# Kernel optimization log

Measured on AMD Instinct MI355X. Metric: run time of the kernel, lower is better.

Reference implementation:

```python
import jax, jax.numpy as jnp
import numpy as np

B, S, H = 4, 4096, 2048
E = 64          # num_routed_experts
TOP_K = 8
TEMP = 1.0      # router_temperature


def setup_inputs() -> dict:
    key = jax.random.key(0)
    k1, k2 = jax.random.split(key)
    hidden_states = jax.random.normal(k1, (B, S, H), dtype=jnp.float32)
    # nn.Linear weight: [out_features, in_features] = [E, H]
    gate_w = jax.random.normal(k2, (E, H), dtype=jnp.float32) * (1.0 / np.sqrt(H))
    return {"hidden_states": hidden_states, "gate_w": gate_w}


def reference(hidden_states, gate_w):
    # Gate projection + temperature scaling: [B,S,H] @ [H,E] -> [B,S,E]
    router_logits = jnp.einsum("bsh,eh->bse", hidden_states, gate_w) / TEMP
    # Top-k over experts
    routing_weights, selected_experts = jax.lax.top_k(router_logits, TOP_K)
    # Softmax over the top-k slots in fp32, cast back to input dtype
    routing_weights = jax.nn.softmax(routing_weights.astype(jnp.float32), axis=-1).astype(hidden_states.dtype)
    return router_logits, routing_weights, selected_experts
```

## Files before the change

kernel.cpp:

```cpp
#include <hip/hip_runtime.h>
#include <math.h>

#define HH 2048
#define EE 64
#define TOPK 8
#define NT 16384
#define MT 32
#define KC 16
#define KQR 512
#define NCH 32
#define LS 68

typedef __attribute__((ext_vector_type(8)))  short short8;
typedef __attribute__((ext_vector_type(16))) float f32x16;

static __device__ __forceinline__ void cvt3(const float4& a, const float4& b,
                                            short8& h, short8& m, short8& l)
{
    const float v[8] = {a.x, a.y, a.z, a.w, b.x, b.y, b.z, b.w};
#pragma unroll
    for (int i = 0; i < 8; ++i) {
        const unsigned int u = __float_as_uint(v[i]);
        h[i] = (short)(u >> 16);
        const float r1 = v[i] - __uint_as_float(u & 0xffff0000u);
        const unsigned int u1 = __float_as_uint(r1);
        m[i] = (short)(u1 >> 16);
        const float r2 = r1 - __uint_as_float(u1 & 0xffff0000u);
        const unsigned int u2 = __float_as_uint(r2);
        l[i] = (short)((u2 + 0x7fffu + ((u2 >> 16) & 1u)) >> 16);
    }
}

__global__ __launch_bounds__(256) void wsplit(
    const float* __restrict__ w, short* __restrict__ wsw)
{
    const int e = blockIdx.x;
    const int o = threadIdx.x;
    const int k = o * 8;
    const float4 a = *(const float4*)(w + (size_t)e * HH + k);
    const float4 b = *(const float4*)(w + (size_t)e * HH + k + 4);
    short8 h, m, l;
    cvt3(a, b, h, m, l);

    const int eb = e >> 5, lr = e & 31;
    const int kq = k >> 9;
    const int c  = (k >> 4) & 31;
    const int l5 = (k >> 3) & 1;
    const int lane = l5 * 32 + lr;
    short* dst = wsw + ((size_t)(((eb * 4 + kq) * 32 + c) * 3) * 64 + lane) * 8;
    *(short8*)(dst)            = h;
    *(short8*)(dst + 64 * 8)   = m;
    *(short8*)(dst + 128 * 8)  = l;
}

__global__ __launch_bounds__(512, 4) void router_fused(
    const float* __restrict__ x,
    const short* __restrict__ wsw,
    float* __restrict__ out_logits,
    float* __restrict__ out_wts,
    float* __restrict__ out_idx)
{
    __shared__ float slog[MT * LS];

    const int t    = threadIdx.x;
    const int wv   = t >> 6;
    const int lane = t & 63;
    const int eb   = wv & 1;
    const int kq   = wv >> 1;
    const int l5   = lane >> 5;
    const int lr   = lane & 31;
    const int tok0 = blockIdx.x * MT;

    const float* xp = x + (size_t)(tok0 + lr) * HH + kq * KQR + l5 * 8;
    const short* wbase = wsw + ((size_t)((eb * 4 + kq) * 32) * 192 + lane) * 8;

    f32x16 accM = {0}, accS = {0};

    short8 wA[3], wB[3];
    float4 xa0, xa1, xb0, xb1;

    auto wload = [&](short8* bw, int c) {
        const short* p0 = wbase + (size_t)c * 1536;
        bw[0] = *(const short8*)(p0);
        bw[1] = *(const short8*)(p0 + 512);
        bw[2] = *(const short8*)(p0 + 1024);
    };
    auto xload = [&](float4& a, float4& b, int c) {
        a = *(const float4*)(xp + c * KC);
        b = *(const float4*)(xp + c * KC + 4);
    };
    auto compute = [&](const float4& a, const float4& b, const short8* bw) {
        short8 xh, xm, xl;
        cvt3(a, b, xh, xm, xl);
        accM = __builtin_amdgcn_mfma_f32_32x32x16_bf16(xh, bw[0], accM, 0, 0, 0);
        accS = __builtin_amdgcn_mfma_f32_32x32x16_bf16(xh, bw[1], accS, 0, 0, 0);
        accS = __builtin_amdgcn_mfma_f32_32x32x16_bf16(xm, bw[0], accS, 0, 0, 0);
        accS = __builtin_amdgcn_mfma_f32_32x32x16_bf16(xh, bw[2], accS, 0, 0, 0);
        accS = __builtin_amdgcn_mfma_f32_32x32x16_bf16(xl, bw[0], accS, 0, 0, 0);
        accS = __builtin_amdgcn_mfma_f32_32x32x16_bf16(xm, bw[1], accS, 0, 0, 0);
    };

    wload(wA, 0); xload(xa0, xa1, 0);
    wload(wB, 1); xload(xb0, xb1, 1);

#pragma unroll 1
    for (int c = 0; c < NCH; c += 2) {
        compute(xa0, xa1, wA);
        if (c + 2 < NCH) { wload(wA, c + 2); xload(xa0, xa1, c + 2); }
        compute(xb0, xb1, wB);
        if (c + 3 < NCH) { wload(wB, c + 3); xload(xb0, xb1, c + 3); }
    }

    const int col = eb * 32 + lr;
#pragma unroll 1
    for (int q = 0; q < 4; ++q) {
        if (kq == q) {
#pragma unroll
            for (int r = 0; r < 16; ++r) {
                const int row = (r & 3) + 8 * (r >> 2) + 4 * l5;
                const float val = accM[r] + accS[r];
                if (q == 0) slog[row * LS + col] = val;
                else        slog[row * LS + col] += val;
            }
        }
        __syncthreads();
    }

    {
        const int row = t >> 4;
        const int c4  = (t & 15) * 4;
        const float4 o0 = *(const float4*)&slog[row * LS + c4];
        *(float4*)(out_logits + (size_t)(tok0 + row) * EE + c4) = o0;
    }

    if (t < MT) {
        float tv[TOPK];
        int   ti[TOPK];
#pragma unroll
        for (int q = 0; q < TOPK; ++q) { tv[q] = -INFINITY; ti[q] = 0; }

        for (int e = 0; e < EE; ++e) {
            const float val = slog[t * LS + e];
            if (val > tv[TOPK - 1]) {
                tv[TOPK - 1] = val;
                ti[TOPK - 1] = e;
#pragma unroll
                for (int q = TOPK - 1; q > 0; --q) {
                    if (tv[q] > tv[q - 1]) {
                        float fv = tv[q]; tv[q] = tv[q - 1]; tv[q - 1] = fv;
                        int   fi = ti[q]; ti[q] = ti[q - 1]; ti[q - 1] = fi;
                    }
                }
            }
        }

        const float m = tv[0];
        float ew[TOPK];
        float sum = 0.f;
#pragma unroll
        for (int q = 0; q < TOPK; ++q) { ew[q] = expf(tv[q] - m); sum += ew[q]; }
        const float inv = 1.f / sum;

        const size_t tok = (size_t)(tok0 + t);
        float4 w0, w1, i0, i1;
        w0.x = ew[0] * inv; w0.y = ew[1] * inv; w0.z = ew[2] * inv; w0.w = ew[3] * inv;
        w1.x = ew[4] * inv; w1.y = ew[5] * inv; w1.z = ew[6] * inv; w1.w = ew[7] * inv;
        i0.x = (float)ti[0]; i0.y = (float)ti[1]; i0.z = (float)ti[2]; i0.w = (float)ti[3];
        i1.x = (float)ti[4]; i1.y = (float)ti[5]; i1.z = (float)ti[6]; i1.w = (float)ti[7];
        *(float4*)(out_wts + tok * TOPK)     = w0;
        *(float4*)(out_wts + tok * TOPK + 4) = w1;
        *(float4*)(out_idx + tok * TOPK)     = i0;
        *(float4*)(out_idx + tok * TOPK + 4) = i1;
    }
}

extern "C" void kernel_launch(void* const* d_in, const int* in_sizes, int n_in,
                              void* d_out, int out_size, void* d_ws, size_t ws_size,
                              hipStream_t stream) {
    const float* x = (const float*)d_in[0];
    const float* w = (const float*)d_in[1];
    float* out        = (float*)d_out;
    float* out_logits = out;
    float* out_wts    = out + (size_t)NT * EE;
    float* out_idx    = out_wts + (size_t)NT * TOPK;
    short* wsw = (short*)d_ws;

    hipLaunchKernelGGL(wsplit, dim3(EE), dim3(256), 0, stream, w, wsw);
    hipLaunchKernelGGL(router_fused, dim3(NT / MT), dim3(512), 0, stream,
                       x, wsw, out_logits, out_wts, out_idx);
}
```

Baseline: 233.8 us.

## Stage x tiles in shared memory so fp32 split is done once per tile

Before, the two expert-half waves that share a k-quarter each loaded x and ran the three-way bf16 split themselves, so every x element was converted twice. Now all 512 threads cooperatively load a 128-wide K chunk of x, split it once, and store the three parts in a double-buffered, XOR-swizzled LDS tile. Waves read their MFMA A operands from LDS, and the weight layout is reorganised into 16-wide K slices to match. The cost is a __syncthreads per chunk and LDS traffic in place of register-resident x, which may reduce how well global loads overlap with MFMA work.

```diff
diff --git a/kernel.cpp b/kernel.cpp
--- a/kernel.cpp
+++ b/kernel.cpp
@@ -6,9 +6,8 @@
 #define TOPK 8
 #define NT 16384
 #define MT 32
-#define KC 16
-#define KQR 512
-#define NCH 32
+#define KC 128
+#define NCH 16
 #define LS 68
 
 typedef __attribute__((ext_vector_type(8)))  short short8;
@@ -42,15 +41,14 @@
     short8 h, m, l;
     cvt3(a, b, h, m, l);
 
-    const int eb = e >> 5, lr = e & 31;
-    const int kq = k >> 9;
-    const int c  = (k >> 4) & 31;
-    const int l5 = (k >> 3) & 1;
+    const int eb  = e >> 5, lr = e & 31;
+    const int s16 = o >> 1;
+    const int l5  = o & 1;
     const int lane = l5 * 32 + lr;
-    short* dst = wsw + ((size_t)(((eb * 4 + kq) * 32 + c) * 3) * 64 + lane) * 8;
-    *(short8*)(dst)            = h;
-    *(short8*)(dst + 64 * 8)   = m;
-    *(short8*)(dst + 128 * 8)  = l;
+    short* dst = wsw + (((size_t)(eb * 128 + s16) * 3) * 64 + lane) * 8;
+    *(short8*)(dst)           = h;
+    *(short8*)(dst + 64 * 8)  = m;
+    *(short8*)(dst + 128 * 8) = l;
 }
 
 __global__ __launch_bounds__(512, 4) void router_fused(
@@ -60,7 +58,8 @@
     float* __restrict__ out_wts,
     float* __restrict__ out_idx)
 {
-    __shared__ float slog[MT * LS];
+    __shared__ __align__(16) short8 xsl[2][1536];
+    float* slog = (float*)xsl;
 
     const int t    = threadIdx.x;
     const int wv   = t >> 6;
@@ -71,44 +70,60 @@
     const int lr   = lane & 31;
     const int tok0 = blockIdx.x * MT;
 
-    const float* xp = x + (size_t)(tok0 + lr) * HH + kq * KQR + l5 * 8;
-    const short* wbase = wsw + ((size_t)((eb * 4 + kq) * 32) * 192 + lane) * 8;
+    const int sr = t >> 4;
+    const int su = t & 15;
+    const float* xg = x + (size_t)(tok0 + sr) * HH + su * 8;
+    const int s16s = su >> 1;
+    const int lfs  = (su & 1) * 32 + sr;
 
     f32x16 accM = {0}, accS = {0};
-
-    short8 wA[3], wB[3];
-    float4 xa0, xa1, xb0, xb1;
-
-    auto wload = [&](short8* bw, int c) {
-        const short* p0 = wbase + (size_t)c * 1536;
-        bw[0] = *(const short8*)(p0);
-        bw[1] = *(const short8*)(p0 + 512);
-        bw[2] = *(const short8*)(p0 + 1024);
+    float4 xr0, xr1;
+
+    auto sload = [&](int c) {
+        xr0 = *(const float4*)(xg + (size_t)c * KC);
+        xr1 = *(const float4*)(xg + (size_t)c * KC + 4);
     };
-    auto xload = [&](float4& a, float4& b, int c) {
-        a = *(const float4*)(xp + c * KC);
-        b = *(const float4*)(xp + c * KC + 4);
+    auto swrite = [&](int buf) {
+        short8 h, m, l;
+        cvt3(xr0, xr1, h, m, l);
+        const int b0 = s16s * 3;
+        xsl[buf][((b0 + 0) << 6) + (lfs ^ ((b0 + 0) & 7))] = h;
+        xsl[buf][((b0 + 1) << 6) + (lfs ^ ((b0 + 1) & 7))] = m;
+        xsl[buf][((b0 + 2) << 6) + (lfs ^ ((b0 + 2) & 7))] = l;
     };
-    auto compute = [&](const float4& a, const float4& b, const short8* bw) {
-        short8 xh, xm, xl;
-        cvt3(a, b, xh, xm, xl);
-        accM = __builtin_amdgcn_mfma_f32_32x32x16_bf16(xh, bw[0], accM, 0, 0, 0);
-        accS = __builtin_amdgcn_mfma_f32_32x32x16_bf16(xh, bw[1], accS, 0, 0, 0);
-        accS = __builtin_amdgcn_mfma_f32_32x32x16_bf16(xm, bw[0], accS, 0, 0, 0);
-        accS = __builtin_amdgcn_mfma_f32_32x32x16_bf16(xh, bw[2], accS, 0, 0, 0);
-        accS = __builtin_amdgcn_mfma_f32_32x32x16_bf16(xl, bw[0], accS, 0, 0, 0);
-        accS = __builtin_amdgcn_mfma_f32_32x32x16_bf16(xm, bw[1], accS, 0, 0, 0);
+    auto chunk = [&](int c, int buf) {
+#pragma unroll
+        for (int st = 0; st < 2; ++st) {
+            const int s16l = kq * 2 + st;
+            const int s16g = c * 8 + s16l;
+            const short8* wp = (const short8*)wsw
+                             + ((size_t)(eb * 128 + s16g) * 3) * 64 + lane;
+            const short8 B0 = wp[0];
+            const short8 B1 = wp[64];
+            const short8 B2 = wp[128];
+            const int ab = s16l * 3;
+            const short8 Ah = xsl[buf][((ab + 0) << 6) + (lane ^ ((ab + 0) & 7))];
+            const short8 Am = xsl[buf][((ab + 1) << 6) + (lane ^ ((ab + 1) & 7))];
+            const short8 Al = xsl[buf][((ab + 2) << 6) + (lane ^ ((ab + 2) & 7))];
+            accM = __builtin_amdgcn_mfma_f32_32x32x16_bf16(Ah, B0, accM, 0, 0, 0);
+            accS = __builtin_amdgcn_mfma_f32_32x32x16_bf16(Ah, B1, accS, 0, 0, 0);
+            accS = __builtin_amdgcn_mfma_f32_32x32x16_bf16(Am, B0, accS, 0, 0, 0);
+            accS = __builtin_amdgcn_mfma_f32_32x32x16_bf16(Ah, B2, accS, 0, 0, 0);
+            accS = __builtin_amdgcn_mfma_f32_32x32x16_bf16(Al, B0, accS, 0, 0, 0);
+            accS = __builtin_amdgcn_mfma_f32_32x32x16_bf16(Am, B1, accS, 0, 0, 0);
+        }
     };
 
-    wload(wA, 0); xload(xa0, xa1, 0);
-    wload(wB, 1); xload(xb0, xb1, 1);
+    sload(0);
+    swrite(0);
+    __syncthreads();
 
 #pragma unroll 1
-    for (int c = 0; c < NCH; c += 2) {
-        compute(xa0, xa1, wA);
-        if (c + 2 < NCH) { wload(wA, c + 2); xload(xa0, xa1, c + 2); }
-        compute(xb0, xb1, wB);
-        if (c + 3 < NCH) { wload(wB, c + 3); xload(xb0, xb1, c + 3); }
+    for (int c = 0; c < NCH; ++c) {
+        if (c + 1 < NCH) sload(c + 1);
+        chunk(c, c & 1);
+        if (c + 1 < NCH) swrite((c + 1) & 1);
+        __syncthreads();
     }
 
     const int col = eb * 32 + lr;
```

Result: faster. 219.8 us (-6.0%).
